# Kernel optimization log

Hardware: AMD Instinct MI355X
Metric: run time of the kernel (lower is better)

## Reference

```python
import jax, jax.numpy as jnp
import numpy as np

HEADS = 16
DIM_HEAD = 64
SCALE = DIM_HEAD ** -0.5
LN_EPS = 1e-5


def setup_inputs() -> dict:
    key = jax.random.key(0)
    ks = jax.random.split(key, 4)
    B, N, D = 2, 2048, 1024
    inner = HEADS * DIM_HEAD  # 1024
    x = jax.random.normal(ks[0], (B, N, D), dtype=jnp.float32)
    m = jax.random.normal(ks[1], (B, N, N), dtype=jnp.float32)
    gamma = jnp.ones((D,), dtype=jnp.float32)
    beta = jnp.zeros((D,), dtype=jnp.float32)
    W_qkv = jax.random.normal(ks[2], (D, 3 * inner), dtype=jnp.float32) * (D ** -0.5)
    W_out = jax.random.normal(ks[3], (inner, D), dtype=jnp.float32) * (inner ** -0.5)
    return {"x": x, "m": m, "gamma": gamma, "beta": beta, "W_qkv": W_qkv, "W_out": W_out}


def reference(x, m, gamma, beta, W_qkv, W_out):
    B, N, D = x.shape
    # LayerNorm
    mu = jnp.mean(x, axis=-1, keepdims=True)
    var = jnp.var(x, axis=-1, keepdims=True)
    xn = (x - mu) * jax.lax.rsqrt(var + LN_EPS) * gamma + beta
    # QKV projection (no bias)
    qkv = xn @ W_qkv  # [B, N, 3*inner]
    q, k, v = jnp.split(qkv, 3, axis=-1)
    split_heads = lambda t: t.reshape(B, N, HEADS, DIM_HEAD).transpose(0, 2, 1, 3)  # b h n d
    q, k, v = split_heads(q), split_heads(k), split_heads(v)
    # Non-standard order: mask added BEFORE scaling
    qk = jnp.einsum('bhid,bhjd->bhij', q, k)
    dots = (qk + m[:, None, :, :]) * SCALE
    attn = jax.nn.softmax(dots, axis=-1)
    out = jnp.einsum('bhij,bhjd->bhid', attn, v)
    out = out.transpose(0, 2, 1, 3).reshape(B, N, HEADS * DIM_HEAD)
    return out @ W_out  # dropout is identity at inference
```

## Files before the change

### kernel.cpp

```cpp
#include <hip/hip_runtime.h>
#include <hip/hip_bf16.h>
#include <math.h>

typedef _Float16 f16;
typedef __fp16 hf2 __attribute__((ext_vector_type(2)));
typedef _Float16 f16x4 __attribute__((ext_vector_type(4)));
typedef _Float16 f16x8 __attribute__((ext_vector_type(8)));
typedef float f32x4 __attribute__((ext_vector_type(4)));
typedef float f32x16 __attribute__((ext_vector_type(16)));
typedef unsigned int u32x2 __attribute__((ext_vector_type(2)));

#define HD 64
#define NH 16
#define BATCH 2
#define SEQ 2048
#define DMODEL 1024
#define NQKV 3072
#define ROWS 4096
#define NEG_BIG (-1.0e30f)
#define SCALE_LOG2E 0.18033688011112042f

__device__ __forceinline__ f32x4 mfma16h(f16x8 a, f16x8 b, f32x4 c){
  return __builtin_amdgcn_mfma_f32_16x16x32_f16(a, b, c, 0, 0, 0);
}
__device__ __forceinline__ f32x16 mfma32h(f16x8 a, f16x8 b, f32x16 c){
  return __builtin_amdgcn_mfma_f32_32x32x16_f16(a, b, c, 0, 0, 0);
}
__device__ __forceinline__ u32x2 pswap(unsigned a, unsigned b){
  return __builtin_amdgcn_permlane32_swap(a, b, false, false);
}
__device__ __forceinline__ unsigned pk16(float a, float b){
  hf2 r = __builtin_amdgcn_cvt_pkrtz(a, b);
  return __builtin_bit_cast(unsigned, r);
}

__device__ __forceinline__ void gload16(const f16* g, f16* l){
  __builtin_amdgcn_global_load_lds(
      (const __attribute__((address_space(1))) unsigned int*)(g),
      (__attribute__((address_space(3))) unsigned int*)(l), 16, 0, 0);
}
__device__ __forceinline__ void gload16f(const float* g, float* l){
  __builtin_amdgcn_global_load_lds(
      (const __attribute__((address_space(1))) unsigned int*)(g),
      (__attribute__((address_space(3))) unsigned int*)(l), 16, 0, 0);
}

__global__ __launch_bounds__(256) void ln_kernel(const float* __restrict__ x,
    const float* __restrict__ gamma, const float* __restrict__ beta,
    f16* __restrict__ xn)
{
  int row = blockIdx.x;
  int tid = threadIdx.x;
  float4 v = ((const float4*)(x + (size_t)row * DMODEL))[tid];
  float s  = v.x + v.y + v.z + v.w;
  float s2 = v.x*v.x + v.y*v.y + v.z*v.z + v.w*v.w;
  #pragma unroll
  for (int off = 32; off; off >>= 1){ s += __shfl_xor(s, off); s2 += __shfl_xor(s2, off); }
  __shared__ float red[8];
  int wave = tid >> 6, lane = tid & 63;
  if (lane == 0){ red[wave] = s; red[4 + wave] = s2; }
  __syncthreads();
  s  = red[0] + red[1] + red[2] + red[3];
  s2 = red[4] + red[5] + red[6] + red[7];
  float mu  = s * (1.f / DMODEL);
  float var = s2 * (1.f / DMODEL) - mu * mu;
  float rs  = rsqrtf(var + 1e-5f);
  float4 g  = ((const float4*)gamma)[tid];
  float4 be = ((const float4*)beta)[tid];
  f16x4 o;
  o[0] = (f16)((v.x - mu) * rs * g.x + be.x);
  o[1] = (f16)((v.y - mu) * rs * g.y + be.y);
  o[2] = (f16)((v.z - mu) * rs * g.z + be.z);
  o[3] = (f16)((v.w - mu) * rs * g.w + be.w);
  *(f16x4*)(xn + (size_t)row * DMODEL + tid*4) = o;
}

__global__ __launch_bounds__(256) void transpose_f2h_kernel(const float* __restrict__ in,
    f16* __restrict__ out, int R, int C)
{
  __shared__ float t[32][33];
  int c0 = blockIdx.x * 32, r0 = blockIdx.y * 32;
  int lx = threadIdx.x & 31, ly = threadIdx.x >> 5;
  #pragma unroll
  for (int i = 0; i < 32; i += 8) t[ly + i][lx] = in[(size_t)(r0 + ly + i) * C + c0 + lx];
  __syncthreads();
  #pragma unroll
  for (int i = 0; i < 32; i += 8) out[(size_t)(c0 + ly + i) * R + r0 + lx] = (f16)t[lx][ly + i];
}

__global__ __launch_bounds__(256, 3) void gemm_qkv(const f16* __restrict__ A,
    const f16* __restrict__ Bt, f16* __restrict__ Qo, f16* __restrict__ Ko,
    f16* __restrict__ Vo)
{
  __shared__ __align__(16) f16 As[2][128][32];
  __shared__ __align__(16) f16 Bs[2][128][32];
  const int K = DMODEL;
  int bm = blockIdx.y * 128, bn = blockIdx.x * 128;
  int tid = threadIdx.x;
  int wave = tid >> 6, lane = tid & 63, quad = lane >> 4, l15 = lane & 15;
  int mw = (wave >> 1) * 64, nw = (wave & 1) * 64;

  int sr0 = wave*16 + (lane >> 2);
  int sr1 = sr0 + 64;
  int sc  = (lane & 3) ^ (sr0 & 3);
  const f16* Ag = A  + (size_t)bm * K;
  const f16* Bg = Bt + (size_t)bn * K;
  f16* ldsA0 = &As[0][wave*16     ][0];
  f16* ldsA1 = &As[0][wave*16 + 64][0];
  f16* ldsB0 = &Bs[0][wave*16     ][0];
  f16* ldsB1 = &Bs[0][wave*16 + 64][0];

#define QSTAGE(buf, k0) do{ \
    gload16(Ag + (size_t)sr0 * K + (k0) + sc*8, ldsA0 + (buf)*4096); \
    gload16(Ag + (size_t)sr1 * K + (k0) + sc*8, ldsA1 + (buf)*4096); \
    gload16(Bg + (size_t)sr0 * K + (k0) + sc*8, ldsB0 + (buf)*4096); \
    gload16(Bg + (size_t)sr1 * K + (k0) + sc*8, ldsB1 + (buf)*4096); }while(0)

  f32x4 zero = {0.f, 0.f, 0.f, 0.f};
  f32x4 acc[4][4];
  #pragma unroll
  for (int i = 0; i < 4; i++)
    #pragma unroll
    for (int j = 0; j < 4; j++) acc[i][j] = zero;

  QSTAGE(0, 0);
  const int NS = K / 32;
  for (int it = 0; it < NS; ++it){
    int cur = it & 1;
    asm volatile("s_waitcnt vmcnt(0)" ::: "memory");
    __syncthreads();
    if (it + 1 < NS) QSTAGE(cur ^ 1, (it + 1) * 32);
    int ca = (quad ^ (l15 & 3)) * 8;
    f16x8 af[4], bfr[4];
    #pragma unroll
    for (int i = 0; i < 4; i++) af[i]  = *(const f16x8*)&As[cur][mw + i*16 + l15][ca];
    #pragma unroll
    for (int i = 0; i < 4; i++) bfr[i] = *(const f16x8*)&Bs[cur][nw + i*16 + l15][ca];
    __builtin_amdgcn_s_setprio(1);
    #pragma unroll
    for (int mi = 0; mi < 4; mi++)
      #pragma unroll
      for (int ni = 0; ni < 4; ni++)
        acc[mi][ni] = mfma16h(af[mi], bfr[ni], acc[mi][ni]);
    __builtin_amdgcn_s_setprio(0);
  }
#undef QSTAGE

  #pragma unroll
  for (int mi = 0; mi < 4; mi++){
    #pragma unroll
    for (int ni = 0; ni < 4; ni++){
      int c = bn + nw + ni*16 + l15;
      int which = c >> 10;
      int hc = c & 1023;
      int h = hc >> 6, d = hc & 63;
      if (which == 2){
        int r = bm + mw + mi*16 + quad*4;
        int b = r >> 11, nseq = r & 2047;
        size_t bh = (size_t)(b * NH + h);
        f16x4 vv;
        #pragma unroll
        for (int reg = 0; reg < 4; reg++) vv[reg] = (f16)acc[mi][ni][reg];
        *(f16x4*)(Vo + (bh * HD + d) * SEQ + nseq) = vv;
      } else {
        #pragma unroll
        for (int reg = 0; reg < 4; reg++){
          int r = bm + mw + mi*16 + quad*4 + reg;
          float v = acc[mi][ni][reg];
          int b = r >> 11, nseq = r & 2047;
          size_t bh = (size_t)(b * NH + h);
          if (which == 0) Qo[(bh * SEQ + nseq) * HD + d] = (f16)(v * SCALE_LOG2E);
          else            Ko[(bh * SEQ + nseq) * HD + d] = (f16)v;
        }
      }
    }
  }
}

__global__ __launch_bounds__(256, 4) void gemm_out(const f16* __restrict__ A,
    const f16* __restrict__ Bt, float* __restrict__ C, int M, int N, int K)
{
  __shared__ __align__(16) f16 As[2][64][32];
  __shared__ __align__(16) f16 Bs[2][128][32];
  int bm = blockIdx.y * 64, bn = blockIdx.x * 128;
  int tid = threadIdx.x;
  int wave = tid >> 6, lane = tid & 63, quad = lane >> 4, l15 = lane & 15;
  int mw = (wave >> 1) * 32, nw = (wave & 1) * 64;

  int sr0 = wave*16 + (lane >> 2);
  int sc  = (lane & 3) ^ (sr0 & 3);
  const f16* Ag = A  + (size_t)bm * K;
  const f16* Bg = Bt + (size_t)bn * K;
  f16* ldsA0 = &As[0][wave*16     ][0];
  f16* ldsB0 = &Bs[0][wave*16     ][0];
  f16* ldsB1 = &Bs[0][wave*16 + 64][0];

#define OSTAGE(buf, k0) do{ \
    gload16(Ag + (size_t)sr0 * K + (k0) + sc*8, ldsA0 + (buf)*2048); \
    gload16(Bg + (size_t)sr0 * K + (k0) + sc*8, ldsB0 + (buf)*4096); \
    gload16(Bg + (size_t)(sr0 + 64) * K + (k0) + sc*8, ldsB1 + (buf)*4096); }while(0)

  f32x4 zero = {0.f, 0.f, 0.f, 0.f};
  f32x4 acc[2][4];
  #pragma unroll
  for (int i = 0; i < 2; i++)
    #pragma unroll
    for (int j = 0; j < 4; j++) acc[i][j] = zero;

  OSTAGE(0, 0);
  const int NS = DMODEL / 32;
  for (int it = 0; it < NS; ++it){
    int cur = it & 1;
    asm volatile("s_waitcnt vmcnt(0)" ::: "memory");
    __syncthreads();
    if (it + 1 < NS) OSTAGE(cur ^ 1, (it + 1) * 32);
    int ca = (quad ^ (l15 & 3)) * 8;
    f16x8 af[2], bfr[4];
    #pragma unroll
    for (int i = 0; i < 2; i++) af[i]  = *(const f16x8*)&As[cur][mw + i*16 + l15][ca];
    #pragma unroll
    for (int i = 0; i < 4; i++) bfr[i] = *(const f16x8*)&Bs[cur][nw + i*16 + l15][ca];
    __builtin_amdgcn_s_setprio(1);
    #pragma unroll
    for (int mi = 0; mi < 2; mi++)
      #pragma unroll
      for (int ni = 0; ni < 4; ni++)
        acc[mi][ni] = mfma16h(af[mi], bfr[ni], acc[mi][ni]);
    __builtin_amdgcn_s_setprio(0);
  }
#undef OSTAGE

  #pragma unroll
  for (int mi = 0; mi < 2; mi++)
    #pragma unroll
    for (int ni = 0; ni < 4; ni++)
      #pragma unroll
      for (int reg = 0; reg < 4; reg++){
        int r = bm + mw + mi*16 + quad*4 + reg;
        int c = bn + nw + ni*16 + l15;
        C[(size_t)r * N + c] = acc[mi][ni][reg];
      }
}

__global__ __launch_bounds__(256, 2) void attn_kernel(const f16* __restrict__ Q,
    const f16* __restrict__ Kb, const f16* __restrict__ Vt,
    const float* __restrict__ mask, f16* __restrict__ Ao)
{
  __shared__ __align__(16) f16 KsB[2][64*64];
  __shared__ __align__(16) f16 VsB[2][64*64];
  __shared__ __align__(16) float Msk[4][2048];

  int bh = blockIdx.y; int b = bh >> 4; int h = bh & 15;
  int q0 = blockIdx.x * 128;
  int tid = threadIdx.x;
  int wave = tid >> 6, lane = tid & 63;
  int l31 = lane & 31, hi = lane >> 5;

  int rA = (wave*2 + 0)*8 + (lane >> 3);
  int rB = (wave*2 + 1)*8 + (lane >> 3);
  int cp = lane & 7;
  int ccA = cp ^ (rA & 7);
  int ccB = cp ^ (rB & 7);
  const f16* Kg = Kb + (size_t)bh * SEQ * HD;
  const f16* Vg = Vt + (size_t)bh * HD * SEQ;
  f16* ldsKA = &KsB[0][0] + (wave*2 + 0)*8*64;
  f16* ldsKB = &KsB[0][0] + (wave*2 + 1)*8*64;
  f16* ldsVA = &VsB[0][0] + (wave*2 + 0)*8*64;
  f16* ldsVB = &VsB[0][0] + (wave*2 + 1)*8*64;

  float* mslab = &Msk[wave][0];
  const float* Mg = mask + ((size_t)b * SEQ + q0 + wave*32) * SEQ;
  int mrl = lane >> 4;
  int msl = lane & 15;

  f16x8 qb[4];
  {
    const f16* qrow = Q + ((size_t)bh * SEQ + q0 + wave*32 + l31) * HD + hi*8;
    #pragma unroll
    for (int kt = 0; kt < 4; kt++) qb[kt] = *(const f16x8*)(qrow + kt*16);
  }

  gload16(Kg + (size_t)(0 + rA)*HD + ccA*8, ldsKA);
  gload16(Kg + (size_t)(0 + rB)*HD + ccB*8, ldsKB);
  gload16(Vg + (size_t)rA*SEQ + 0 + ccA*8, ldsVA);
  gload16(Vg + (size_t)rB*SEQ + 0 + ccB*8, ldsVB);

  f32x16 O0, O1;
  #pragma unroll
  for (int i = 0; i < 16; i++){ O0[i] = 0.f; O1[i] = 0.f; }
  float mrun = NEG_BIG, lrun = 0.f;

  const int NT = SEQ / 64;
  for (int it = 0; it < NT; ++it){
    int cur = it & 1;
    int j0 = it * 64;
    asm volatile("s_waitcnt vmcnt(0)" ::: "memory");
    __syncthreads();

    #pragma unroll
    for (int t = 0; t < 8; t++){
      int r = t*4 + mrl;
      gload16f(Mg + (size_t)r * SEQ + j0 + ((msl ^ (r & 15)) << 2), mslab + t*256);
    }
    {
      int nb = cur ^ 1;
      int jn = (j0 + 64) & (SEQ - 1);
      gload16(Kg + (size_t)(jn + rA)*HD + ccA*8, ldsKA + nb*4096);
      gload16(Kg + (size_t)(jn + rB)*HD + ccB*8, ldsKB + nb*4096);
      gload16(Vg + (size_t)rA*SEQ + jn + ccA*8, ldsVA + nb*4096);
      gload16(Vg + (size_t)rB*SEQ + jn + ccB*8, ldsVB + nb*4096);
    }
    const f16* Ksc = &KsB[cur][0];
    const f16* Vsc = &VsB[cur][0];

    f32x16 s0, s1;
    #pragma unroll
    for (int i = 0; i < 16; i++){ s0[i] = 0.f; s1[i] = 0.f; }
    __builtin_amdgcn_s_setprio(1);
    #pragma unroll
    for (int kt = 0; kt < 4; kt++){
      int c = ((kt*2 + hi) ^ (l31 & 7)) * 8;
      f16x8 ka0 = *(const f16x8*)&Ksc[ l31      *64 + c];
      f16x8 ka1 = *(const f16x8*)&Ksc[(32 + l31)*64 + c];
      s0 = mfma32h(ka0, qb[kt], s0);
      s1 = mfma32h(ka1, qb[kt], s1);
    }
    __builtin_amdgcn_s_setprio(0);

    asm volatile("s_waitcnt vmcnt(4)" ::: "memory");

    float p0[16], p1[16];
    #pragma unroll
    for (int g = 0; g < 4; g++){
      float4 mv0 = *(const float4*)&Msk[wave][l31*64 + ((( g*2 + hi) ^ (l31 & 15)) << 2)];
      float4 mv1 = *(const float4*)&Msk[wave][l31*64 + (((8 + g*2 + hi) ^ (l31 & 15)) << 2)];
      p0[g*4+0] = fmaf(mv0.x, SCALE_LOG2E, s0[g*4+0]);
      p0[g*4+1] = fmaf(mv0.y, SCALE_LOG2E, s0[g*4+1]);
      p0[g*4+2] = fmaf(mv0.z, SCALE_LOG2E, s0[g*4+2]);
      p0[g*4+3] = fmaf(mv0.w, SCALE_LOG2E, s0[g*4+3]);
      p1[g*4+0] = fmaf(mv1.x, SCALE_LOG2E, s1[g*4+0]);
      p1[g*4+1] = fmaf(mv1.y, SCALE_LOG2E, s1[g*4+1]);
      p1[g*4+2] = fmaf(mv1.z, SCALE_LOG2E, s1[g*4+2]);
      p1[g*4+3] = fmaf(mv1.w, SCALE_LOG2E, s1[g*4+3]);
    }

    float t0 = fmaxf(fmaxf(fmaxf(p0[0],p0[1]),fmaxf(p0[2],p0[3])),
                     fmaxf(fmaxf(p0[4],p0[5]),fmaxf(p0[6],p0[7])));
    float t1 = fmaxf(fmaxf(fmaxf(p0[8],p0[9]),fmaxf(p0[10],p0[11])),
                     fmaxf(fmaxf(p0[12],p0[13]),fmaxf(p0[14],p0[15])));
    float t2 = fmaxf(fmaxf(fmaxf(p1[0],p1[1]),fmaxf(p1[2],p1[3])),
                     fmaxf(fmaxf(p1[4],p1[5]),fmaxf(p1[6],p1[7])));
    float t3 = fmaxf(fmaxf(fmaxf(p1[8],p1[9]),fmaxf(p1[10],p1[11])),
                     fmaxf(fmaxf(p1[12],p1[13]),fmaxf(p1[14],p1[15])));
    float tmax = fmaxf(fmaxf(t0, t1), fmaxf(t2, t3));
    {
      u32x2 r = pswap(__float_as_uint(tmax), __float_as_uint(tmax));
      tmax = fmaxf(__uint_as_float(r[0]), __uint_as_float(r[1]));
    }

    if (__any(tmax > mrun + 8.f)){
      float nm = fmaxf(mrun, tmax);
      float alpha = exp2f(mrun - nm);
      mrun = nm;
      lrun *= alpha;
      #pragma unroll
      for (int i = 0; i < 16; i++){ O0[i] *= alpha; O1[i] *= alpha; }
    }

    float ps = 0.f;
    #pragma unroll
    for (int i = 0; i < 16; i++){
      p0[i] = exp2f(p0[i] - mrun); ps += p0[i];
      p1[i] = exp2f(p1[i] - mrun); ps += p1[i];
    }
    lrun += ps;

    unsigned u0[4][2], u1[4][2];
    #pragma unroll
    for (int g = 0; g < 4; g++){
      u0[g][0] = pk16(p0[g*4+0], p0[g*4+1]);
      u0[g][1] = pk16(p0[g*4+2], p0[g*4+3]);
      u1[g][0] = pk16(p1[g*4+0], p1[g*4+1]);
      u1[g][1] = pk16(p1[g*4+2], p1[g*4+3]);
    }
    f16x8 pb[4];
    #pragma unroll
    for (int m = 0; m < 2; m++){
      u32x2 r0 = pswap(u0[2*m][0], u0[2*m+1][0]);
      u32x2 r1 = pswap(u0[2*m][1], u0[2*m+1][1]);
      union { unsigned u[4]; f16x8 v; } w;
      w.u[0] = r0[0]; w.u[1] = r1[0]; w.u[2] = r0[1]; w.u[3] = r1[1];
      pb[m] = w.v;
      r0 = pswap(u1[2*m][0], u1[2*m+1][0]);
      r1 = pswap(u1[2*m][1], u1[2*m+1][1]);
      w.u[0] = r0[0]; w.u[1] = r1[0]; w.u[2] = r0[1]; w.u[3] = r1[1];
      pb[2 + m] = w.v;
    }

    __builtin_amdgcn_s_setprio(1);
    #pragma unroll
    for (int jt = 0; jt < 4; jt++){
      int c = ((jt*2 + hi) ^ (l31 & 7)) * 8;
      f16x8 va0 = *(const f16x8*)&Vsc[ l31      *64 + c];
      f16x8 va1 = *(const f16x8*)&Vsc[(32 + l31)*64 + c];
      O0 = mfma32h(va0, pb[jt], O0);
      O1 = mfma32h(va1, pb[jt], O1);
    }
    __builtin_amdgcn_s_setprio(0);
  }

  {
    u32x2 r = pswap(__float_as_uint(lrun), __float_as_uint(lrun));
    lrun = __uint_as_float(r[0]) + __uint_as_float(r[1]);
  }
  float inv = 1.0f / lrun;
  f16* slab = (f16*)&Msk[wave][0];
  #pragma unroll
  for (int g = 0; g < 4; g++){
    f16x4 w0, w1;
    #pragma unroll
    for (int rg = 0; rg < 4; rg++){
      w0[rg] = (f16)(O0[g*4+rg] * inv);
      w1[rg] = (f16)(O1[g*4+rg] * inv);
    }
    *(f16x4*)&slab[l31*72 +      g*8 + hi*4] = w0;
    *(f16x4*)&slab[l31*72 + 32 + g*8 + hi*4] = w1;
  }
  int ir  = lane >> 3;
  int c16 = lane & 7;
  #pragma unroll
  for (int rr = 0; rr < 4; rr++){
    int i = rr*8 + ir;
    f16x8 ov = *(const f16x8*)&slab[i*72 + c16*8];
    *(f16x8*)(Ao + ((size_t)(b * SEQ + q0 + wave*32 + i)) * DMODEL + h * HD + c16*8) = ov;
  }
}

extern "C" void kernel_launch(void* const* d_in, const int* in_sizes, int n_in,
                              void* d_out, int out_size, void* d_ws, size_t ws_size,
                              hipStream_t stream)
{
  (void)in_sizes; (void)n_in; (void)out_size; (void)ws_size;
  const float* x     = (const float*)d_in[0];
  const float* m     = (const float*)d_in[1];
  const float* gamma = (const float*)d_in[2];
  const float* beta  = (const float*)d_in[3];
  const float* Wqkv  = (const float*)d_in[4];
  const float* Wout  = (const float*)d_in[5];
  float* out = (float*)d_out;

  char* ws = (char*)d_ws;
  f16* xn    = (f16*)(ws + 0);
  f16* Ao    = (f16*)(ws + 0);
  f16* Qb    = (f16*)(ws + 8388608);
  f16* WoutT = (f16*)(ws + 8388608);
  f16* Kbuf  = (f16*)(ws + 16777216);
  f16* Vtb   = (f16*)(ws + 25165824);
  f16* WqkvT = (f16*)(ws + 33554432);

  ln_kernel<<<ROWS, 256, 0, stream>>>(x, gamma, beta, xn);
  transpose_f2h_kernel<<<dim3(NQKV/32, DMODEL/32), 256, 0, stream>>>(Wqkv, WqkvT, DMODEL, NQKV);
  gemm_qkv<<<dim3(NQKV/128, ROWS/128), 256, 0, stream>>>(xn, WqkvT, Qb, Kbuf, Vtb);
  attn_kernel<<<dim3(SEQ/128, BATCH*NH), 256, 0, stream>>>(Qb, Kbuf, Vtb, m, Ao);
  transpose_f2h_kernel<<<dim3(DMODEL/32, DMODEL/32), 256, 0, stream>>>(Wout, WoutT, DMODEL, DMODEL);
  gemm_out<<<dim3(DMODEL/128, ROWS/64), 256, 0, stream>>>(Ao, WoutT, out, ROWS, DMODEL, DMODEL);
}
```

Baseline: 240.6 us.

## Prefetch next mask tile during softmax and vectorize Q/K stores in QKV GEMM

The attention loop now issues the mask loads for the next KV tile right after the current mask values are consumed, instead of at the top of the iteration behind a full vmcnt(0) wait. The wait at the loop head becomes a partial vmcnt(8) with a raw barrier. This is meant to overlap mask fetch latency with the softmax and PV compute. Separately, the QKV GEMM swaps MFMA operands for Q/K tiles so each lane holds contiguous columns and can write f16x4 vectors instead of scalar halves. The risk is in the wait-count ordering and in the single-buffered mask slab being reused across iterations.

```diff
diff --git a/kernel.cpp b/kernel.cpp
--- a/kernel.cpp
+++ b/kernel.cpp
@@ -125,36 +125,76 @@
 
   QSTAGE(0, 0);
   const int NS = K / 32;
-  for (int it = 0; it < NS; ++it){
-    int cur = it & 1;
-    asm volatile("s_waitcnt vmcnt(0)" ::: "memory");
-    __syncthreads();
-    if (it + 1 < NS) QSTAGE(cur ^ 1, (it + 1) * 32);
-    int ca = (quad ^ (l15 & 3)) * 8;
-    f16x8 af[4], bfr[4];
-    #pragma unroll
-    for (int i = 0; i < 4; i++) af[i]  = *(const f16x8*)&As[cur][mw + i*16 + l15][ca];
-    #pragma unroll
-    for (int i = 0; i < 4; i++) bfr[i] = *(const f16x8*)&Bs[cur][nw + i*16 + l15][ca];
-    __builtin_amdgcn_s_setprio(1);
-    #pragma unroll
-    for (int mi = 0; mi < 4; mi++)
-      #pragma unroll
-      for (int ni = 0; ni < 4; ni++)
-        acc[mi][ni] = mfma16h(af[mi], bfr[ni], acc[mi][ni]);
-    __builtin_amdgcn_s_setprio(0);
-  }
-#undef QSTAGE
-
-  #pragma unroll
-  for (int mi = 0; mi < 4; mi++){
-    #pragma unroll
-    for (int ni = 0; ni < 4; ni++){
-      int c = bn + nw + ni*16 + l15;
-      int which = c >> 10;
-      int hc = c & 1023;
-      int h = hc >> 6, d = hc & 63;
-      if (which == 2){
+  if (bn < 2048){
+    for (int it = 0; it < NS; ++it){
+      int cur = it & 1;
+      asm volatile("s_waitcnt vmcnt(0)" ::: "memory");
+      __syncthreads();
+      if (it + 1 < NS) QSTAGE(cur ^ 1, (it + 1) * 32);
+      int ca = (quad ^ (l15 & 3)) * 8;
+      f16x8 af[4], bfr[4];
+      #pragma unroll
+      for (int i = 0; i < 4; i++) af[i]  = *(const f16x8*)&As[cur][mw + i*16 + l15][ca];
+      #pragma unroll
+      for (int i = 0; i < 4; i++) bfr[i] = *(const f16x8*)&Bs[cur][nw + i*16 + l15][ca];
+      __builtin_amdgcn_s_setprio(1);
+      #pragma unroll
+      for (int mi = 0; mi < 4; mi++)
+        #pragma unroll
+        for (int ni = 0; ni < 4; ni++)
+          acc[mi][ni] = mfma16h(bfr[ni], af[mi], acc[mi][ni]);
+      __builtin_amdgcn_s_setprio(0);
+    }
+    #pragma unroll
+    for (int mi = 0; mi < 4; mi++){
+      int r = bm + mw + mi*16 + l15;
+      int b = r >> 11, nseq = r & 2047;
+      #pragma unroll
+      for (int ni = 0; ni < 4; ni++){
+        int c0 = bn + nw + ni*16 + quad*4;
+        int which = c0 >> 10;
+        int hc = c0 & 1023;
+        int h = hc >> 6, d = hc & 63;
+        size_t bh = (size_t)(b * NH + h);
+        f16x4 o;
+        if (which == 0){
+          #pragma unroll
+          for (int reg = 0; reg < 4; reg++) o[reg] = (f16)(acc[mi][ni][reg] * SCALE_LOG2E);
+          *(f16x4*)(Qo + (bh * SEQ + nseq) * HD + d) = o;
+        } else {
+          #pragma unroll
+          for (int reg = 0; reg < 4; reg++) o[reg] = (f16)acc[mi][ni][reg];
+          *(f16x4*)(Ko + (bh * SEQ + nseq) * HD + d) = o;
+        }
+      }
+    }
+  } else {
+    for (int it = 0; it < NS; ++it){
+      int cur = it & 1;
+      asm volatile("s_waitcnt vmcnt(0)" ::: "memory");
+      __syncthreads();
+      if (it + 1 < NS) QSTAGE(cur ^ 1, (it + 1) * 32);
+      int ca = (quad ^ (l15 & 3)) * 8;
+      f16x8 af[4], bfr[4];
+      #pragma unroll
+      for (int i = 0; i < 4; i++) af[i]  = *(const f16x8*)&As[cur][mw + i*16 + l15][ca];
+      #pragma unroll
+      for (int i = 0; i < 4; i++) bfr[i] = *(const f16x8*)&Bs[cur][nw + i*16 + l15][ca];
+      __builtin_amdgcn_s_setprio(1);
+      #pragma unroll
+      for (int mi = 0; mi < 4; mi++)
+        #pragma unroll
+        for (int ni = 0; ni < 4; ni++)
+          acc[mi][ni] = mfma16h(af[mi], bfr[ni], acc[mi][ni]);
+      __builtin_amdgcn_s_setprio(0);
+    }
+    #pragma unroll
+    for (int mi = 0; mi < 4; mi++){
+      #pragma unroll
+      for (int ni = 0; ni < 4; ni++){
+        int c = bn + nw + ni*16 + l15;
+        int hc = c & 1023;
+        int h = hc >> 6, d = hc & 63;
         int r = bm + mw + mi*16 + quad*4;
         int b = r >> 11, nseq = r & 2047;
         size_t bh = (size_t)(b * NH + h);
@@ -162,19 +202,10 @@
         #pragma unroll
         for (int reg = 0; reg < 4; reg++) vv[reg] = (f16)acc[mi][ni][reg];
         *(f16x4*)(Vo + (bh * HD + d) * SEQ + nseq) = vv;
-      } else {
-        #pragma unroll
-        for (int reg = 0; reg < 4; reg++){
-          int r = bm + mw + mi*16 + quad*4 + reg;
-          float v = acc[mi][ni][reg];
-          int b = r >> 11, nseq = r & 2047;
-          size_t bh = (size_t)(b * NH + h);
-          if (which == 0) Qo[(bh * SEQ + nseq) * HD + d] = (f16)(v * SCALE_LOG2E);
-          else            Ko[(bh * SEQ + nseq) * HD + d] = (f16)v;
-        }
       }
     }
   }
+#undef QSTAGE
 }
 
 __global__ __launch_bounds__(256, 4) void gemm_out(const f16* __restrict__ A,
@@ -273,6 +304,13 @@
   int mrl = lane >> 4;
   int msl = lane & 15;
 
+#define MSTAGE(jj) do{ \
+    _Pragma("unroll") \
+    for (int t = 0; t < 8; t++){ \
+      int r_ = t*4 + mrl; \
+      gload16f(Mg + (size_t)r_ * SEQ + (jj) + ((msl ^ (r_ & 15)) << 2), mslab + t*256); \
+    } }while(0)
+
   f16x8 qb[4];
   {
     const f16* qrow = Q + ((size_t)bh * SEQ + q0 + wave*32 + l31) * HD + hi*8;
@@ -284,6 +322,7 @@
   gload16(Kg + (size_t)(0 + rB)*HD + ccB*8, ldsKB);
   gload16(Vg + (size_t)rA*SEQ + 0 + ccA*8, ldsVA);
   gload16(Vg + (size_t)rB*SEQ + 0 + ccB*8, ldsVB);
+  MSTAGE(0);
 
   f32x16 O0, O1;
   #pragma unroll
@@ -294,17 +333,11 @@
   for (int it = 0; it < NT; ++it){
     int cur = it & 1;
     int j0 = it * 64;
-    asm volatile("s_waitcnt vmcnt(0)" ::: "memory");
-    __syncthreads();
-
-    #pragma unroll
-    for (int t = 0; t < 8; t++){
-      int r = t*4 + mrl;
-      gload16f(Mg + (size_t)r * SEQ + j0 + ((msl ^ (r & 15)) << 2), mslab + t*256);
-    }
+    int jn = (j0 + 64) & (SEQ - 1);
+    asm volatile("s_waitcnt vmcnt(8)" ::: "memory");
+    __builtin_amdgcn_s_barrier();
     {
       int nb = cur ^ 1;
-      int jn = (j0 + 64) & (SEQ - 1);
       gload16(Kg + (size_t)(jn + rA)*HD + ccA*8, ldsKA + nb*4096);
       gload16(Kg + (size_t)(jn + rB)*HD + ccB*8, ldsKB + nb*4096);
       gload16(Vg + (size_t)rA*SEQ + jn + ccA*8, ldsVA + nb*4096);
@@ -343,6 +376,8 @@
       p1[g*4+2] = fmaf(mv1.z, SCALE_LOG2E, s1[g*4+2]);
       p1[g*4+3] = fmaf(mv1.w, SCALE_LOG2E, s1[g*4+3]);
     }
+
+    MSTAGE(jn);
 
     float t0 = fmaxf(fmaxf(fmaxf(p0[0],p0[1]),fmaxf(p0[2],p0[3])),
                      fmaxf(fmaxf(p0[4],p0[5]),fmaxf(p0[6],p0[7])));
@@ -408,7 +443,9 @@
     }
     __builtin_amdgcn_s_setprio(0);
   }
-
+#undef MSTAGE
+
+  asm volatile("s_waitcnt vmcnt(0)" ::: "memory");
   {
     u32x2 r = pswap(__float_as_uint(lrun), __float_as_uint(lrun));
     lrun = __uint_as_float(r[0]) + __uint_as_float(r[1]);
```

Result: no change. 244.1 us (+1.4%).

## Single-buffer K/V tiles and stagger loads to fit three attention blocks per CU

Applied to the files above, without the earlier changes.

Attention K and V staging moves from double-buffered to single-buffered LDS, cutting LDS per block so launch bounds can rise from 2 to 3 blocks per CU. To keep loads overlapped, the loop is re-pipelined: the V tile is loaded at the top of each iteration, the next K tile after QK^T, and the next mask slab after the mask is consumed. Split barriers with partial vmcnt waits replace the single full wait and sync. The intent is higher occupancy to hide memory latency, at the cost of more barriers per iteration, shorter prefetch distance and fragile hand-counted vmcnt values.

```diff
diff --git a/kernel.cpp b/kernel.cpp
--- a/kernel.cpp
+++ b/kernel.cpp
@@ -242,12 +242,12 @@
       }
 }
 
-__global__ __launch_bounds__(256, 2) void attn_kernel(const f16* __restrict__ Q,
+__global__ __launch_bounds__(256, 3) void attn_kernel(const f16* __restrict__ Q,
     const f16* __restrict__ Kb, const f16* __restrict__ Vt,
     const float* __restrict__ mask, f16* __restrict__ Ao)
 {
-  __shared__ __align__(16) f16 KsB[2][64*64];
-  __shared__ __align__(16) f16 VsB[2][64*64];
+  __shared__ __align__(16) f16 Ks[64*64];
+  __shared__ __align__(16) f16 Vs[64*64];
   __shared__ __align__(16) float Msk[4][2048];
 
   int bh = blockIdx.y; int b = bh >> 4; int h = bh & 15;
@@ -263,16 +263,23 @@
   int ccB = cp ^ (rB & 7);
   const f16* Kg = Kb + (size_t)bh * SEQ * HD;
   const f16* Vg = Vt + (size_t)bh * HD * SEQ;
-  f16* ldsKA = &KsB[0][0] + (wave*2 + 0)*8*64;
-  f16* ldsKB = &KsB[0][0] + (wave*2 + 1)*8*64;
-  f16* ldsVA = &VsB[0][0] + (wave*2 + 0)*8*64;
-  f16* ldsVB = &VsB[0][0] + (wave*2 + 1)*8*64;
+  f16* ldsKA = &Ks[0] + (wave*2 + 0)*8*64;
+  f16* ldsKB = &Ks[0] + (wave*2 + 1)*8*64;
+  f16* ldsVA = &Vs[0] + (wave*2 + 0)*8*64;
+  f16* ldsVB = &Vs[0] + (wave*2 + 1)*8*64;
 
   float* mslab = &Msk[wave][0];
   const float* Mg = mask + ((size_t)b * SEQ + q0 + wave*32) * SEQ;
   int mrl = lane >> 4;
   int msl = lane & 15;
 
+#define MSTAGE(jj) do{ \
+    _Pragma("unroll") \
+    for (int t = 0; t < 8; t++){ \
+      int r_ = t*4 + mrl; \
+      gload16f(Mg + (size_t)r_ * SEQ + (jj) + ((msl ^ (r_ & 15)) << 2), mslab + t*256); \
+    } }while(0)
+
   f16x8 qb[4];
   {
     const f16* qrow = Q + ((size_t)bh * SEQ + q0 + wave*32 + l31) * HD + hi*8;
@@ -282,8 +289,7 @@
 
   gload16(Kg + (size_t)(0 + rA)*HD + ccA*8, ldsKA);
   gload16(Kg + (size_t)(0 + rB)*HD + ccB*8, ldsKB);
-  gload16(Vg + (size_t)rA*SEQ + 0 + ccA*8, ldsVA);
-  gload16(Vg + (size_t)rB*SEQ + 0 + ccB*8, ldsVB);
+  MSTAGE(0);
 
   f32x16 O0, O1;
   #pragma unroll
@@ -292,26 +298,13 @@
 
   const int NT = SEQ / 64;
   for (int it = 0; it < NT; ++it){
-    int cur = it & 1;
     int j0 = it * 64;
-    asm volatile("s_waitcnt vmcnt(0)" ::: "memory");
-    __syncthreads();
-
-    #pragma unroll
-    for (int t = 0; t < 8; t++){
-      int r = t*4 + mrl;
-      gload16f(Mg + (size_t)r * SEQ + j0 + ((msl ^ (r & 15)) << 2), mslab + t*256);
-    }
-    {
-      int nb = cur ^ 1;
-      int jn = (j0 + 64) & (SEQ - 1);
-      gload16(Kg + (size_t)(jn + rA)*HD + ccA*8, ldsKA + nb*4096);
-      gload16(Kg + (size_t)(jn + rB)*HD + ccB*8, ldsKB + nb*4096);
-      gload16(Vg + (size_t)rA*SEQ + jn + ccA*8, ldsVA + nb*4096);
-      gload16(Vg + (size_t)rB*SEQ + jn + ccB*8, ldsVB + nb*4096);
-    }
-    const f16* Ksc = &KsB[cur][0];
-    const f16* Vsc = &VsB[cur][0];
+    int jn = (j0 + 64) & (SEQ - 1);
+
+    asm volatile("s_waitcnt vmcnt(8)" ::: "memory");
+    __builtin_amdgcn_s_barrier();
+    gload16(Vg + (size_t)rA*SEQ + j0 + ccA*8, ldsVA);
+    gload16(Vg + (size_t)rB*SEQ + j0 + ccB*8, ldsVB);
 
     f32x16 s0, s1;
     #pragma unroll
@@ -320,12 +313,16 @@
     #pragma unroll
     for (int kt = 0; kt < 4; kt++){
       int c = ((kt*2 + hi) ^ (l31 & 7)) * 8;
-      f16x8 ka0 = *(const f16x8*)&Ksc[ l31      *64 + c];
-      f16x8 ka1 = *(const f16x8*)&Ksc[(32 + l31)*64 + c];
+      f16x8 ka0 = *(const f16x8*)&Ks[ l31      *64 + c];
+      f16x8 ka1 = *(const f16x8*)&Ks[(32 + l31)*64 + c];
       s0 = mfma32h(ka0, qb[kt], s0);
       s1 = mfma32h(ka1, qb[kt], s1);
     }
     __builtin_amdgcn_s_setprio(0);
+
+    __builtin_amdgcn_s_barrier();
+    gload16(Kg + (size_t)(jn + rA)*HD + ccA*8, ldsKA);
+    gload16(Kg + (size_t)(jn + rB)*HD + ccB*8, ldsKB);
 
     asm volatile("s_waitcnt vmcnt(4)" ::: "memory");
 
@@ -343,6 +340,8 @@
       p1[g*4+2] = fmaf(mv1.z, SCALE_LOG2E, s1[g*4+2]);
       p1[g*4+3] = fmaf(mv1.w, SCALE_LOG2E, s1[g*4+3]);
     }
+
+    MSTAGE(jn);
 
     float t0 = fmaxf(fmaxf(fmaxf(p0[0],p0[1]),fmaxf(p0[2],p0[3])),
                      fmaxf(fmaxf(p0[4],p0[5]),fmaxf(p0[6],p0[7])));
@@ -397,18 +396,23 @@
       pb[2 + m] = w.v;
     }
 
+    asm volatile("s_waitcnt vmcnt(10)" ::: "memory");
+    __builtin_amdgcn_s_barrier();
+
     __builtin_amdgcn_s_setprio(1);
     #pragma unroll
     for (int jt = 0; jt < 4; jt++){
       int c = ((jt*2 + hi) ^ (l31 & 7)) * 8;
-      f16x8 va0 = *(const f16x8*)&Vsc[ l31      *64 + c];
-      f16x8 va1 = *(const f16x8*)&Vsc[(32 + l31)*64 + c];
+      f16x8 va0 = *(const f16x8*)&Vs[ l31      *64 + c];
+      f16x8 va1 = *(const f16x8*)&Vs[(32 + l31)*64 + c];
       O0 = mfma32h(va0, pb[jt], O0);
       O1 = mfma32h(va1, pb[jt], O1);
     }
     __builtin_amdgcn_s_setprio(0);
   }
-
+#undef MSTAGE
+
+  asm volatile("s_waitcnt vmcnt(0)" ::: "memory");
   {
     u32x2 r = pswap(__float_as_uint(lrun), __float_as_uint(lrun));
     lrun = __uint_as_float(r[0]) + __uint_as_float(r[1]);
```

Measured after the change: 244.6 us. About the same (+1.7%).
